# Kernel optimization log

Hardware: AMD Instinct MI355X
Metric: run time of the kernel (lower is better)

## Reference

```python
import jax, jax.numpy as jnp
import numpy as np
import math

HIDDEN = 1024
HEADS = 16
HEAD_DIM = HIDDEN // HEADS
B, S = 4, 2048


def setup_inputs() -> dict:
    key = jax.random.key(0)
    ks = jax.random.split(key, 10)
    x = jax.random.normal(ks[0], (B, S, HIDDEN), dtype=jnp.float32)
    time_intervals = jax.random.uniform(ks[1], (B, S, S), dtype=jnp.float32)
    mask = jax.random.randint(ks[2], (B, 1, S, S), 0, 2, dtype=jnp.int32)
    scale = 1.0 / math.sqrt(HIDDEN)
    Wq = jax.random.normal(ks[3], (HIDDEN, HIDDEN), dtype=jnp.float32) * scale
    bq = jnp.zeros((HIDDEN,), dtype=jnp.float32)
    Wk = jax.random.normal(ks[4], (HIDDEN, HIDDEN), dtype=jnp.float32) * scale
    bk = jnp.zeros((HIDDEN,), dtype=jnp.float32)
    Wv = jax.random.normal(ks[5], (HIDDEN, HIDDEN), dtype=jnp.float32) * scale
    bv = jnp.zeros((HIDDEN,), dtype=jnp.float32)
    alpha = jnp.asarray(0.1, dtype=jnp.float32)
    return {"x": x, "time_intervals": time_intervals, "mask": mask,
            "Wq": Wq, "bq": bq, "Wk": Wk, "bk": bk, "Wv": Wv, "bv": bv,
            "alpha": alpha}


def reference(x, time_intervals, mask, Wq, bq, Wk, bk, Wv, bv, alpha):
    b, s, _ = x.shape
    # projections -> [b, heads, s, head_dim]
    def proj(W, bias):
        y = x @ W + bias
        return y.reshape(b, s, HEADS, HEAD_DIM).transpose(0, 2, 1, 3)
    Q = proj(Wq, bq)
    K = proj(Wk, bk)
    V = proj(Wv, bv)
    scores = jnp.einsum('bhqd,bhkd->bhqk', Q, K) / math.sqrt(HEAD_DIM)
    # additive time-decay bias, broadcast over heads
    scores = scores + (-jnp.abs(alpha)) * time_intervals[:, None, :, :]
    scores = jnp.where(mask == 0, jnp.float32(-1e9), scores)
    attn = jax.nn.softmax(scores, axis=-1)
    out = jnp.einsum('bhqk,bhkd->bhqd', attn, V)
    return out.transpose(0, 2, 1, 3).reshape(b, s, HIDDEN)
```

## Files before the change

### kernel.cpp

```cpp
#include <hip/hip_runtime.h>
#include <hip/hip_bf16.h>
#include <hip/hip_fp16.h>

#define BATCH 4
#define SEQ   2048
#define HID   1024
#define HEADS 16
#define HDIM  64
#define MROWS (BATCH * SEQ)
#define LOG2E 1.4426950408889634f
#define SCL   (LOG2E / 8.0f)

typedef _Float16 v8h __attribute__((ext_vector_type(8)));
typedef _Float16 v4h __attribute__((ext_vector_type(4)));
typedef _Float16 v2h __attribute__((ext_vector_type(2)));
typedef float    v4f __attribute__((ext_vector_type(4)));
typedef int      v4i __attribute__((ext_vector_type(4)));

#define MFMA16(a, b, c) __builtin_amdgcn_mfma_f32_16x16x32_f16((a), (b), (c), 0, 0, 0)
#define MFMA16K16(a, b, c) __builtin_amdgcn_mfma_f32_16x16x16f16((a), (b), (c), 0, 0, 0)

__device__ inline int pk2(float a, float b) {
    return __builtin_bit_cast(int, __builtin_amdgcn_cvt_pkrtz(a, b));
}

__device__ __forceinline__ void async16(const void* g, void* l) {
    __builtin_amdgcn_global_load_lds(
        (const __attribute__((address_space(1))) unsigned int*)g,
        (__attribute__((address_space(3))) unsigned int*)l, 16, 0, 0);
}

#define SWZ(row, chunk) (((row) * 64) + ((((chunk) ^ ((row) & 7))) * 8))

__global__ __launch_bounds__(256) void prep(
    const float* __restrict__ x, _Float16* __restrict__ xb,
    const float* __restrict__ W0, const float* __restrict__ W1,
    const float* __restrict__ W2, _Float16* __restrict__ Wt) {
    __shared__ float t[32][33];
    const int bid = blockIdx.x;
    const int tid = threadIdx.x;
    if (bid < 4096) {
        int i = bid * 256 + tid;
        const float4* xp = (const float4*)x;
        float4 a = xp[2 * i];
        float4 b = xp[2 * i + 1];
        v4i o;
        o[0] = pk2(a.x, a.y); o[1] = pk2(a.z, a.w);
        o[2] = pk2(b.x, b.y); o[3] = pk2(b.z, b.w);
        ((v4i*)xb)[i] = o;
    } else {
        int tt = bid - 4096;
        int z = tt >> 10;
        int rem = tt & 1023;
        const float* W = (z == 0) ? W0 : (z == 1 ? W1 : W2);
        _Float16* dst = Wt + (size_t)z * HID * HID;
        int bx = (rem & 31) * 32, by = (rem >> 5) * 32;
        int tx = tid & 31, ty = tid >> 5;
#pragma unroll
        for (int i = 0; i < 4; i++)
            t[ty + i * 8][tx] = W[(size_t)(by + ty + i * 8) * HID + bx + tx];
        __syncthreads();
#pragma unroll
        for (int i = 0; i < 4; i++)
            dst[(size_t)(bx + ty + i * 8) * HID + by + tx] = (_Float16)t[tx][ty + i * 8];
    }
}

__global__ __launch_bounds__(256) void gemm_bias(
    const _Float16* __restrict__ xb, const _Float16* __restrict__ wt,
    const float* __restrict__ bq, const float* __restrict__ bk,
    const float* __restrict__ bv,
    _Float16* __restrict__ Qb, _Float16* __restrict__ Kb, _Float16* __restrict__ Vtb,
    const float* __restrict__ tiv, const int* __restrict__ msk,
    const float* __restrict__ alphap, _Float16* __restrict__ biasT) {
    __shared__ _Float16 smem[2 * 128 * 64];
    const int bid = blockIdx.x;
    const int tid = threadIdx.x;

    if (bid < 1536) {
        const int mode = bid >> 9;
        const int within = bid & 511;
        const int n0 = (within & 7) * 128;
        const int m0 = (within >> 3) * 128;
        const _Float16* w = wt + (size_t)mode * HID * HID;
        _Float16* As = smem;
        _Float16* Bs = smem + 128 * 64;
        const int wv = tid >> 6, lane = tid & 63;
        const int quad = lane >> 4, l15 = lane & 15;
        const int wr = wv >> 1, wc = wv & 1;

        v4f acc[4][4];
#pragma unroll
        for (int i = 0; i < 4; i++)
#pragma unroll
            for (int j = 0; j < 4; j++) acc[i][j] = (v4f){0.f, 0.f, 0.f, 0.f};

        const int srow = lane >> 3;
        const int schk = lane & 7;
        const _Float16* Ag = xb + (size_t)m0 * HID;
        const _Float16* Bg = w + (size_t)n0 * HID;

        for (int k0 = 0; k0 < HID; k0 += 64) {
            __syncthreads();
#pragma unroll
            for (int i = 0; i < 4; i++) {
                int ra = wv * 32 + i * 8 + srow;
                int ca = schk ^ (ra & 7);
                async16(Ag + (size_t)ra * HID + k0 + ca * 8, &As[(wv * 32 + i * 8) * 64]);
                async16(Bg + (size_t)ra * HID + k0 + ca * 8, &Bs[(wv * 32 + i * 8) * 64]);
            }
            __syncthreads();
#pragma unroll
            for (int kc = 0; kc < 2; kc++) {
                v8h af[4], bf[4];
#pragma unroll
                for (int t = 0; t < 4; t++) {
                    af[t] = *(const v8h*)&As[SWZ(wr * 64 + t * 16 + l15, kc * 4 + quad)];
                    bf[t] = *(const v8h*)&Bs[SWZ(wc * 64 + t * 16 + l15, kc * 4 + quad)];
                }
#pragma unroll
                for (int tm = 0; tm < 4; tm++)
#pragma unroll
                    for (int tn = 0; tn < 4; tn++)
                        acc[tm][tn] = MFMA16(af[tm], bf[tn], acc[tm][tn]);
            }
        }

        const float* pb = (mode == 0) ? bq : (mode == 1 ? bk : bv);
        const float oscl = (mode == 0) ? SCL : 1.0f;
#pragma unroll
        for (int tm = 0; tm < 4; tm++) {
#pragma unroll
            for (int tn = 0; tn < 4; tn++) {
                int n = n0 + wc * 64 + tn * 16 + l15;
                float bval = pb[n];
                int h = n >> 6, d = n & 63;
#pragma unroll
                for (int r = 0; r < 4; r++) {
                    int m = m0 + wr * 64 + tm * 16 + quad * 4 + r;
                    int b = m >> 11, s = m & 2047;
                    _Float16 hv = (_Float16)((acc[tm][tn][r] + bval) * oscl);
                    if (mode == 2) {
                        Vtb[(((size_t)(b * HEADS + h) * HDIM + d) * SEQ) + s] = hv;
                    } else {
                        _Float16* dst = (mode == 0) ? Qb : Kb;
                        dst[((size_t)(b * HEADS + h) * SEQ + s) * HDIM + d] = hv;
                    }
                }
            }
        }
    } else {
        const int t = bid - 1536;
        const int kc0 = (t & 7) * 256;
        const int Q16 = (t >> 3) & 127;
        const int b = t >> 10;
        _Float16* L = smem;
        const float ca = -fabsf(alphap[0]) * LOG2E;
        const int prow = tid >> 6;
        const int pcol = (tid & 63) * 4;
#pragma unroll
        for (int pi = 0; pi < 4; pi++) {
            int r = pi * 4 + prow;
            size_t g = ((size_t)b * SEQ + Q16 * 16 + r) * SEQ + kc0 + pcol;
            float4 tv = *(const float4*)(tiv + g);
            int4   mv = *(const int4*)(msk + g);
            float f0 = mv.x ? ca * tv.x : -57344.0f;
            float f1 = mv.y ? ca * tv.y : -57344.0f;
            float f2 = mv.z ? ca * tv.z : -57344.0f;
            float f3 = mv.w ? ca * tv.w : -57344.0f;
            int2 o; o.x = pk2(f0, f1); o.y = pk2(f2, f3);
            *(int2*)&L[r * 264 + pcol] = o;
        }
        __syncthreads();
        const int lane = tid & 63, tq = tid >> 6;
#pragma unroll
        for (int it = 0; it < 4; it++) {
            int K16i = it * 4 + tq;
            int kl = K16i * 16 + (lane >> 4) * 4;
            int qr = lane & 15;
            int2 v = *(const int2*)&L[qr * 264 + kl];
            size_t o = ((((size_t)b * 128 + (kc0 >> 4) + K16i) * 128 + Q16) * 64 + lane) * 4;
            *(int2*)&biasT[o] = v;
        }
    }
}

__global__ __launch_bounds__(256, 4) void attn(
    const _Float16* __restrict__ Qb, const _Float16* __restrict__ Kb,
    const _Float16* __restrict__ Vtb, const _Float16* __restrict__ biasT,
    float* __restrict__ out) {
    const int wg  = (blockIdx.y << 4) | blockIdx.x;
    const int nid = ((wg & 7) << 7) | (wg >> 3);
    const int bh = nid >> 4;
    const int qt = nid & 15;
    const int b = bh >> 4, h = bh & 15;
    const int tid = threadIdx.x;
    const int wv = tid >> 6, lane = tid & 63;
    const int quad = lane >> 4, l15 = lane & 15;

    __shared__ _Float16 Ks[2][64 * 64];
    __shared__ _Float16 Vs[2][64 * 64];

    const int q0 = qt * 128 + wv * 32;
    const int Q16a = q0 >> 4;

    const _Float16* Qp = Qb + (size_t)(b * HEADS + h) * SEQ * HDIM;
    const _Float16* Kp = Kb + (size_t)(b * HEADS + h) * SEQ * HDIM;
    const _Float16* Vp = Vtb + (size_t)(b * HEADS + h) * HDIM * SEQ;
    const _Float16* Bbase = biasT + (size_t)b * 128 * 128 * 64 * 4;

    v8h qf[2][2];
#pragma unroll
    for (int tm = 0; tm < 2; tm++)
#pragma unroll
        for (int kc = 0; kc < 2; kc++)
            qf[tm][kc] = *(const v8h*)&Qp[(size_t)(q0 + tm * 16 + l15) * HDIM + kc * 32 + quad * 8];

    v4f oacc[2][4];
#pragma unroll
    for (int i = 0; i < 2; i++)
#pragma unroll
        for (int j = 0; j < 4; j++) oacc[i][j] = (v4f){0.f, 0.f, 0.f, 0.f};
    float lsum[2] = {0.f, 0.f};

    const int srow = lane >> 3, schk = lane & 7;

#define STAGE(buf_, key0_)                                                  \
    {                                                                       \
        _Pragma("unroll")                                                   \
        for (int i_ = 0; i_ < 2; i_++) {                                    \
            int r_ = wv * 16 + i_ * 8 + srow;                               \
            int c_ = schk ^ (r_ & 7);                                       \
            async16(Kp + (size_t)((key0_) + r_) * HDIM + c_ * 8,            \
                    &Ks[buf_][(wv * 16 + i_ * 8) * 64]);                    \
            async16(Vp + (size_t)r_ * SEQ + (key0_) + c_ * 8,               \
                    &Vs[buf_][(wv * 16 + i_ * 8) * 64]);                    \
        }                                                                   \
    }

#define BLOAD(key0_)                                                        \
    {                                                                       \
        _Pragma("unroll")                                                   \
        for (int nt_ = 0; nt_ < 4; nt_++)                                   \
            _Pragma("unroll")                                               \
            for (int tm_ = 0; tm_ < 2; tm_++)                               \
                bl[nt_][tm_] = *(const int2*)&Bbase[((((size_t)((key0_) >> 4) + nt_) * 128 + Q16a + tm_) * 64 + lane) * 4]; \
    }

    int2 bl[4][2];
    STAGE(0, 0)
    BLOAD(0)
    __syncthreads();

    for (int kt = 0; kt < SEQ / 64; kt++) {
        const int cur = kt & 1;
        const int key0 = kt * 64;

        v4f sacc[4][2];
#pragma unroll
        for (int nt = 0; nt < 4; nt++)
#pragma unroll
            for (int tm = 0; tm < 2; tm++) {
                v4h bv = __builtin_bit_cast(v4h, bl[nt][tm]);
                sacc[nt][tm] = (v4f){(float)bv[0], (float)bv[1], (float)bv[2], (float)bv[3]};
            }

        if (kt + 1 < SEQ / 64) {
            STAGE(cur ^ 1, key0 + 64)
            BLOAD(key0 + 64)
        }

#pragma unroll
        for (int kc = 0; kc < 2; kc++) {
            v8h kfr[4];
#pragma unroll
            for (int nt = 0; nt < 4; nt++)
                kfr[nt] = *(const v8h*)&Ks[cur][SWZ(nt * 16 + l15, kc * 4 + quad)];
#pragma unroll
            for (int nt = 0; nt < 4; nt++)
#pragma unroll
                for (int tm = 0; tm < 2; tm++)
                    sacc[nt][tm] = MFMA16(kfr[nt], qf[tm][kc], sacc[nt][tm]);
        }

        int2 pfr[4][2];
#pragma unroll
        for (int nt = 0; nt < 4; nt++)
#pragma unroll
            for (int tm = 0; tm < 2; tm++) {
                float p0 = __builtin_amdgcn_exp2f(sacc[nt][tm][0]);
                float p1 = __builtin_amdgcn_exp2f(sacc[nt][tm][1]);
                float p2 = __builtin_amdgcn_exp2f(sacc[nt][tm][2]);
                float p3 = __builtin_amdgcn_exp2f(sacc[nt][tm][3]);
                int2 pkv;
                pkv.x = pk2(p0, p1);
                pkv.y = pk2(p2, p3);
                lsum[tm] += (p0 + p1) + (p2 + p3);
                pfr[nt][tm] = pkv;
            }

#pragma unroll
        for (int g = 0; g < 4; g++) {
            v4h vfr[4];
#pragma unroll
            for (int nt = 0; nt < 4; nt++) {
                int row = nt * 16 + l15;
                int cc = g * 2 + (quad >> 1);
                vfr[nt] = *(const v4h*)&Vs[cur][row * 64 + ((cc ^ (row & 7)) * 8) + (quad & 1) * 4];
            }
#pragma unroll
            for (int tm = 0; tm < 2; tm++) {
                v4h pa = __builtin_bit_cast(v4h, pfr[g][tm]);
#pragma unroll
                for (int nt = 0; nt < 4; nt++)
                    oacc[tm][nt] = MFMA16K16(pa, vfr[nt], oacc[tm][nt]);
            }
        }

        __syncthreads();
    }

#undef STAGE
#undef BLOAD

#pragma unroll
    for (int tm = 0; tm < 2; tm++) {
        float lt = lsum[tm];
        lt += __shfl_xor(lt, 16);
        lt += __shfl_xor(lt, 32);
        float inv[4];
#pragma unroll
        for (int r = 0; r < 4; r++)
            inv[r] = 1.0f / __shfl(lt, quad * 4 + r);
#pragma unroll
        for (int nt = 0; nt < 4; nt++)
#pragma unroll
            for (int r = 0; r < 4; r++) {
                int q = q0 + tm * 16 + quad * 4 + r;
                int d = nt * 16 + l15;
                out[((size_t)b * SEQ + q) * HID + h * HDIM + d] = oacc[tm][nt][r] * inv[r];
            }
    }
}

extern "C" void kernel_launch(void* const* d_in, const int* in_sizes, int n_in,
                              void* d_out, int out_size, void* d_ws, size_t ws_size,
                              hipStream_t stream) {
    const float* x    = (const float*)d_in[0];
    const float* tiv  = (const float*)d_in[1];
    const int*   msk  = (const int*)d_in[2];
    const float* Wq   = (const float*)d_in[3];
    const float* bq   = (const float*)d_in[4];
    const float* Wk   = (const float*)d_in[5];
    const float* bk   = (const float*)d_in[6];
    const float* Wv   = (const float*)d_in[7];
    const float* bv   = (const float*)d_in[8];
    const float* alp  = (const float*)d_in[9];

    char* ws = (char*)d_ws;
    const size_t XB_OFF = 0;
    const size_t WT_OFF = XB_OFF + (size_t)MROWS * HID * 2;
    const size_t Q_OFF  = WT_OFF + (size_t)3 * HID * HID * 2;
    const size_t K_OFF  = Q_OFF + (size_t)MROWS * HID * 2;
    const size_t V_OFF  = K_OFF + (size_t)MROWS * HID * 2;
    const size_t B_OFF  = V_OFF + (size_t)MROWS * HID * 2;

    _Float16* xb   = (_Float16*)(ws + XB_OFF);
    _Float16* wt   = (_Float16*)(ws + WT_OFF);
    _Float16* Qb   = (_Float16*)(ws + Q_OFF);
    _Float16* Kb   = (_Float16*)(ws + K_OFF);
    _Float16* Vtb  = (_Float16*)(ws + V_OFF);
    _Float16* bias = (_Float16*)(ws + B_OFF);

    prep<<<4096 + 3072, 256, 0, stream>>>(x, xb, Wq, Wk, Wv, wt);
    gemm_bias<<<1536 + 4096, 256, 0, stream>>>(xb, wt, bq, bk, bv, Qb, Kb, Vtb,
                                               tiv, msk, alp, bias);
    attn<<<dim3(SEQ / 128, BATCH * HEADS), 256, 0, stream>>>(Qb, Kb, Vtb, bias,
                                                             (float*)d_out);
}
```

Baseline: 376.5 us.

## Double-buffer QKV projection GEMM tiles and remap block order

The projection GEMM now keeps two LDS buffers and issues async loads for the next K-slice while MFMAs run on the current one, with one barrier per iteration instead of two. Block IDs are also remapped so consecutive blocks work on different mode/tile combinations, changing cache locality and how work spreads across CUs. Doubling LDS to 64KB per block may reduce occupancy. The async load completion wait relies on the single barrier, which is only safe if async16 or the barrier waits on vmcnt.

```diff
diff --git a/kernel.cpp b/kernel.cpp
--- a/kernel.cpp
+++ b/kernel.cpp
@@ -73,18 +73,19 @@
     _Float16* __restrict__ Qb, _Float16* __restrict__ Kb, _Float16* __restrict__ Vtb,
     const float* __restrict__ tiv, const int* __restrict__ msk,
     const float* __restrict__ alphap, _Float16* __restrict__ biasT) {
-    __shared__ _Float16 smem[2 * 128 * 64];
+    __shared__ _Float16 smem[2 * 2 * 128 * 64];
     const int bid = blockIdx.x;
     const int tid = threadIdx.x;
 
     if (bid < 1536) {
-        const int mode = bid >> 9;
-        const int within = bid & 511;
+        const int nid = (bid & 7) * 192 + (bid >> 3);
+        const int mode = nid >> 9;
+        const int within = nid & 511;
         const int n0 = (within & 7) * 128;
         const int m0 = (within >> 3) * 128;
         const _Float16* w = wt + (size_t)mode * HID * HID;
-        _Float16* As = smem;
-        _Float16* Bs = smem + 128 * 64;
+        _Float16 (*As)[128 * 64] = (_Float16(*)[128 * 64])smem;
+        _Float16 (*Bs)[128 * 64] = (_Float16(*)[128 * 64])(smem + 2 * 128 * 64);
         const int wv = tid >> 6, lane = tid & 63;
         const int quad = lane >> 4, l15 = lane & 15;
         const int wr = wv >> 1, wc = wv & 1;
@@ -100,23 +101,32 @@
         const _Float16* Ag = xb + (size_t)m0 * HID;
         const _Float16* Bg = w + (size_t)n0 * HID;
 
-        for (int k0 = 0; k0 < HID; k0 += 64) {
-            __syncthreads();
-#pragma unroll
-            for (int i = 0; i < 4; i++) {
-                int ra = wv * 32 + i * 8 + srow;
-                int ca = schk ^ (ra & 7);
-                async16(Ag + (size_t)ra * HID + k0 + ca * 8, &As[(wv * 32 + i * 8) * 64]);
-                async16(Bg + (size_t)ra * HID + k0 + ca * 8, &Bs[(wv * 32 + i * 8) * 64]);
-            }
-            __syncthreads();
+#define STAGEG(buf_, k0_)                                                   \
+        {                                                                   \
+            _Pragma("unroll")                                               \
+            for (int i_ = 0; i_ < 4; i_++) {                                \
+                int ra_ = wv * 32 + i_ * 8 + srow;                          \
+                int ca_ = schk ^ (ra_ & 7);                                 \
+                async16(Ag + (size_t)ra_ * HID + (k0_) + ca_ * 8,           \
+                        &As[buf_][(wv * 32 + i_ * 8) * 64]);                \
+                async16(Bg + (size_t)ra_ * HID + (k0_) + ca_ * 8,           \
+                        &Bs[buf_][(wv * 32 + i_ * 8) * 64]);                \
+            }                                                               \
+        }
+
+        STAGEG(0, 0)
+        __syncthreads();
+
+        for (int it = 0; it < HID / 64; it++) {
+            const int cur = it & 1;
+            if (it + 1 < HID / 64) STAGEG(cur ^ 1, (it + 1) * 64)
 #pragma unroll
             for (int kc = 0; kc < 2; kc++) {
                 v8h af[4], bf[4];
 #pragma unroll
                 for (int t = 0; t < 4; t++) {
-                    af[t] = *(const v8h*)&As[SWZ(wr * 64 + t * 16 + l15, kc * 4 + quad)];
-                    bf[t] = *(const v8h*)&Bs[SWZ(wc * 64 + t * 16 + l15, kc * 4 + quad)];
+                    af[t] = *(const v8h*)&As[cur][SWZ(wr * 64 + t * 16 + l15, kc * 4 + quad)];
+                    bf[t] = *(const v8h*)&Bs[cur][SWZ(wc * 64 + t * 16 + l15, kc * 4 + quad)];
                 }
 #pragma unroll
                 for (int tm = 0; tm < 4; tm++)
@@ -124,7 +134,9 @@
                     for (int tn = 0; tn < 4; tn++)
                         acc[tm][tn] = MFMA16(af[tm], bf[tn], acc[tm][tn]);
             }
-        }
+            __syncthreads();
+        }
+#undef STAGEG
 
         const float* pb = (mode == 0) ? bq : (mode == 1 ? bk : bv);
         const float oscl = (mode == 0) ? SCL : 1.0f;
```

After: 364.5 us. 1.03x faster.
